# Kernel optimization log

Measured on AMD Instinct MI355X. Metric: run time of the kernel, lower is better.

Reference implementation:

```python
import jax, jax.numpy as jnp
import numpy as np


def setup_inputs() -> dict:
    key = jax.random.key(0)
    k1, k2 = jax.random.split(key)
    N, C, H, W = 8, 512, 64, 64
    K = 64
    x = jax.random.normal(k1, (N, C, H, W), dtype=jnp.float32)
    y = jax.random.normal(k2, (N, K, H, W), dtype=jnp.float32)
    scale = jnp.zeros((1,), dtype=jnp.float32)
    return {"x": x, "y": y, "scale": scale}


def reference(x, y, scale):
    N, C, H, W = x.shape
    K = y.shape[1]
    HW = H * W
    xq = x.reshape(N, C, HW)            # (N, C, HW) queries (channel-wise)
    yk = y.reshape(N, K, HW)            # (N, K, HW) keys/values
    # energy: (N, C, K)
    energy = jnp.einsum('ncs,nks->nck', xq, yk)
    # inverted max-subtraction: softmax(max_k(E) - E) over last dim
    energy_new = jnp.max(energy, axis=-1, keepdims=True) - energy
    attention = jax.nn.softmax(energy_new, axis=-1)  # (N, C, K)
    out = jnp.einsum('nck,nks->ncs', attention, yk)   # (N, C, HW)
    out = out.reshape(N, C, H, W)
    return x + scale * out
```

## Files before the change

### kernel.cpp

```cpp
#include <hip/hip_runtime.h>

#define N_ 8
#define C_ 512
#define K_ 64
#define HW_ 4096
#define SCHUNK 256
#define NCH 16

typedef __attribute__((ext_vector_type(8))) short short8;
typedef __attribute__((ext_vector_type(4))) float floatx4;

__device__ __forceinline__ short8 cvt8(const float* __restrict__ p){
  float4 u = *(const float4*)p;
  float4 w = *(const float4*)(p + 4);
  union { unsigned u32[4]; short8 s; } r;
  asm("v_cvt_pk_bf16_f32 %0, %1, %2" : "=v"(r.u32[0]) : "v"(u.x), "v"(u.y));
  asm("v_cvt_pk_bf16_f32 %0, %1, %2" : "=v"(r.u32[1]) : "v"(u.z), "v"(u.w));
  asm("v_cvt_pk_bf16_f32 %0, %1, %2" : "=v"(r.u32[2]) : "v"(w.x), "v"(w.y));
  asm("v_cvt_pk_bf16_f32 %0, %1, %2" : "=v"(r.u32[3]) : "v"(w.z), "v"(w.w));
  return r.s;
}

__device__ __forceinline__ void gload16(const void* g, void* l){
  __builtin_amdgcn_global_load_lds(
      (const __attribute__((address_space(1))) void*)g,
      (__attribute__((address_space(3))) void*)l, 16, 0, 0);
}

__global__ __launch_bounds__(256) void k_prep(const float* __restrict__ y,
                                              unsigned short* __restrict__ ybf,
                                              unsigned short* __restrict__ ytr){
  __shared__ unsigned short tile[64][72];
  int n  = blockIdx.x >> 6;
  int s0 = (blockIdx.x & 63) << 6;
  int tid = threadIdx.x;
  int k  = tid >> 2;
  int sc = (tid & 3) << 4;
  const float* yp = y + ((size_t)n * K_ + k) * HW_ + s0 + sc;
  union { unsigned short u16[16]; short8 s8[2]; uint4 q[2]; } u;
  u.s8[0] = cvt8(yp);
  u.s8[1] = cvt8(yp + 8);
  unsigned short* rp = ybf + ((size_t)n * K_ + k) * HW_ + s0 + sc;
  *(uint4*)rp       = u.q[0];
  *(uint4*)(rp + 8) = u.q[1];
#pragma unroll
  for (int j = 0; j < 16; ++j) tile[sc + j][k] = u.u16[j];
  __syncthreads();
  int s  = tid >> 2;
  int kc = (tid & 3) << 4;
  unsigned short* tp = ytr + ((size_t)n * HW_ + s0 + s) * K_ + kc;
  *(uint4*)tp       = *(const uint4*)&tile[s][kc];
  *(uint4*)(tp + 8) = *(const uint4*)&tile[s][kc + 8];
}

__global__ __launch_bounds__(1024) void k_fused(const float* __restrict__ x,
                                                const unsigned short* __restrict__ ybf,
                                                const unsigned short* __restrict__ ytr,
                                                const float* __restrict__ scale,
                                                float* __restrict__ out){
  __shared__ char smem[116736];

  const int bid = ((blockIdx.x & 7) << 5) | (blockIdx.x >> 3);
  const int ct = bid & 31, n = bid >> 5;
  const int tid = threadIdx.x;
  const int w = tid >> 6, l = tid & 63;
  const int lo = l & 15, hi = l >> 4;
  const int h = w >> 2, q = w & 3;
  const int c0 = ct << 4;

  float sc = scale[0];
  asm volatile("" :: "v"(sc));

  const char* asrc = (const char*)(x + ((size_t)n * C_ + c0 + w) * HW_)
                     + ((16 * l) ^ ((w & 7) << 4));
  const int kb = (w << 1) + (l >> 5);
  const char* bsrc0 = (const char*)(ybf + ((size_t)n * K_ + kb) * HW_)
                      + ((16 * (l & 31)) ^ ((kb & 7) << 4));
  const char* bsrc1 = bsrc0 + (size_t)32 * HW_ * 2;

  floatx4 acc = {0.f, 0.f, 0.f, 0.f};
  const int aswz = (lo & 7) << 4;
  const int brow = (q << 4) + lo;

#define AS(BUF) (smem + (BUF) * 49152)
#define BS(BUF) (smem + (BUF) * 49152 + 16384)
#define STAGE(BUF, CH)                                                         \
  {                                                                            \
    gload16(asrc  + (size_t)(CH) * (SCHUNK * 4), AS(BUF) + (w << 10));         \
    gload16(bsrc0 + (size_t)(CH) * (SCHUNK * 2), BS(BUF) + (w << 10));         \
    gload16(bsrc1 + (size_t)(CH) * (SCHUNK * 2), BS(BUF) + 16384 + (w << 10)); \
  }

  STAGE(0, 0)

#pragma unroll
  for (int ch = 0; ch < NCH; ++ch){
    const int cur = ch & 1;
    if (ch + 1 < NCH){
      STAGE(cur ^ 1, ch + 1)
      asm volatile("s_waitcnt vmcnt(3)" ::: "memory");
    } else {
      asm volatile("s_waitcnt vmcnt(0)" ::: "memory");
    }
    __builtin_amdgcn_s_barrier();
    __builtin_amdgcn_sched_barrier(0);
#pragma unroll
    for (int ss = 0; ss < 2; ++ss){
      int ao = (h << 8) + (ss << 7) + (hi << 5);
      const char* ab = AS(cur) + (lo << 10);
      float4 a0f = *(const float4*)(ab + ((ao     ) ^ aswz));
      float4 a1f = *(const float4*)(ab + ((ao + 16) ^ aswz));
      union { unsigned u32[4]; short8 s; } af;
      asm("v_cvt_pk_bf16_f32 %0, %1, %2" : "=v"(af.u32[0]) : "v"(a0f.x), "v"(a0f.y));
      asm("v_cvt_pk_bf16_f32 %0, %1, %2" : "=v"(af.u32[1]) : "v"(a0f.z), "v"(a0f.w));
      asm("v_cvt_pk_bf16_f32 %0, %1, %2" : "=v"(af.u32[2]) : "v"(a1f.x), "v"(a1f.y));
      asm("v_cvt_pk_bf16_f32 %0, %1, %2" : "=v"(af.u32[3]) : "v"(a1f.z), "v"(a1f.w));
      int bo = (h << 7) + (ss << 6) + (hi << 4);
      short8 bfr = *(const short8*)(BS(cur) + brow * 512 + (bo ^ aswz));
      acc = __builtin_amdgcn_mfma_f32_16x16x32_bf16(bfr, af.s, acc, 0, 0, 0);
    }
    __builtin_amdgcn_sched_barrier(0);
    __builtin_amdgcn_s_barrier();
  }
#undef STAGE

  float (*Els)[16][64] = (float (*)[16][64])(smem + 98304);
  *(floatx4*)&Els[h][lo][(q << 4) + (hi << 2)] = acc;
  __syncthreads();

  char* attl = smem + 114688;
  if (tid < 256){
    int c = tid >> 4, j = tid & 15;
    float4 t0 = *(const float4*)&Els[0][c][4 * j];
    float4 t1 = *(const float4*)&Els[1][c][4 * j];
    float4 t2 = *(const float4*)&Els[2][c][4 * j];
    float4 t3 = *(const float4*)&Els[3][c][4 * j];
    float e0 = t0.x + t1.x + t2.x + t3.x;
    float e1 = t0.y + t1.y + t2.y + t3.y;
    float e2 = t0.z + t1.z + t2.z + t3.z;
    float e3 = t0.w + t1.w + t2.w + t3.w;
    float m = fminf(fminf(e0, e1), fminf(e2, e3));
#pragma unroll
    for (int off = 8; off; off >>= 1) m = fminf(m, __shfl_xor(m, off, 16));
    float p0 = __expf(m - e0), p1 = __expf(m - e1);
    float p2 = __expf(m - e2), p3 = __expf(m - e3);
    float s = p0 + p1 + p2 + p3;
#pragma unroll
    for (int off = 8; off; off >>= 1) s += __shfl_xor(s, off, 16);
    float inv = 1.f / s;
    unsigned d0, d1;
    asm("v_cvt_pk_bf16_f32 %0, %1, %2" : "=v"(d0) : "v"(p0 * inv), "v"(p1 * inv));
    asm("v_cvt_pk_bf16_f32 %0, %1, %2" : "=v"(d1) : "v"(p2 * inv), "v"(p3 * inv));
    uint2 dd; dd.x = d0; dd.y = d1;
    *(uint2*)(attl + c * 128 + ((8 * j) ^ ((c & 7) << 4))) = dd;
  }
  __syncthreads();

  short8 batt0 = *(const short8*)(attl + lo * 128 + ((     hi * 16) ^ ((lo & 7) << 4)));
  short8 batt1 = *(const short8*)(attl + lo * 128 + ((64 + hi * 16) ^ ((lo & 7) << 4)));
  const unsigned short* ybn = ytr + (size_t)n * HW_ * K_;
  const int sP = w << 8;
  float (*Tw)[68] = (float (*)[68])(smem + w * 4352);
  size_t xb[4];
#pragma unroll
  for (int rg = 0; rg < 4; ++rg)
    xb[rg] = ((size_t)n * C_ + c0 + (rg << 2) + hi) * HW_ + sP + (lo << 2);

  short8 aA[8]; float4 xA[4];
  short8 aB[8]; float4 xB[4];

#define PVLOAD(G, AV, XV)                                                      \
  {                                                                            \
    int sg = sP + (G) * 64;                                                    \
    _Pragma("unroll")                                                          \
    for (int t = 0; t < 4; ++t){                                               \
      const unsigned short* ap = ybn + (size_t)(sg + t * 16 + lo) * K_ + (hi << 3); \
      AV[2 * t]     = *(const short8*)(ap);                                    \
      AV[2 * t + 1] = *(const short8*)(ap + 32);                               \
    }                                                                          \
    _Pragma("unroll")                                                          \
    for (int rg = 0; rg < 4; ++rg)                                             \
      XV[rg] = *(const float4*)(x + xb[rg] + (G) * 64);                        \
  }

#define PVCOMP(G, AV, XV)                                                      \
  {                                                                            \
    _Pragma("unroll")                                                          \
    for (int t = 0; t < 4; ++t){                                               \
      floatx4 a2 = {0.f, 0.f, 0.f, 0.f};                                       \
      a2 = __builtin_amdgcn_mfma_f32_16x16x32_bf16(AV[2 * t],     batt0, a2, 0, 0, 0); \
      a2 = __builtin_amdgcn_mfma_f32_16x16x32_bf16(AV[2 * t + 1], batt1, a2, 0, 0, 0); \
      *(floatx4*)&Tw[lo][t * 16 + (hi << 2)] = a2;    \
    }                                                                          \
    _Pragma("unroll")                                                          \
    for (int rg = 0; rg < 4; ++rg){                                            \
      float4 v  = *(const float4*)&Tw[(rg << 2) + hi][lo << 2];                \
      float4 xv = XV[rg];                                                      \
      float4 o;                                                                \
      o.x = xv.x + sc * v.x; o.y = xv.y + sc * v.y;                            \
      o.z = xv.z + sc * v.z; o.w = xv.w + sc * v.w;                            \
      *(float4*)(out + xb[rg] + (G) * 64) = o;                                 \
    }                                                                          \
  }

  PVLOAD(0, aA, xA)
  PVLOAD(1, aB, xB)
  PVCOMP(0, aA, xA)
  PVLOAD(2, aA, xA)
  PVCOMP(1, aB, xB)
  PVLOAD(3, aB, xB)
  PVCOMP(2, aA, xA)
  PVCOMP(3, aB, xB)
#undef PVLOAD
#undef PVCOMP
#undef AS
#undef BS
}

extern "C" void kernel_launch(void* const* d_in, const int* in_sizes, int n_in,
                              void* d_out, int out_size, void* d_ws, size_t ws_size,
                              hipStream_t stream){
  const float* x     = (const float*)d_in[0];
  const float* y     = (const float*)d_in[1];
  const float* scale = (const float*)d_in[2];
  float* out = (float*)d_out;

  char* ws = (char*)d_ws;
  unsigned short* ybf = (unsigned short*)(ws);
  unsigned short* ytr = (unsigned short*)(ws + (4u<<20));

  k_prep  <<<N_ * (HW_/64), 256,  0, stream>>>(y, ybf, ytr);
  k_fused <<<N_ * 32,       1024, 0, stream>>>(x, ybf, ytr, scale, out);
}
```

Baseline: 50.64 us.

## Split fused kernel into split-S energy/softmax kernel and separate PV kernel

Replaces the single 1024-thread fused kernel with a split-spatial energy kernel that accumulates partial C×K energies via global atomics, where the last-arriving block computes the softmax and writes bf16 attention to workspace. A separate PV kernel with more, smaller blocks then reads the attention and produces the output. The intent is more blocks and better occupancy across CUs. In exchange it adds a memset, atomics, an extra launch, and a second full read of x.

```diff
diff --git a/kernel.cpp b/kernel.cpp
--- a/kernel.cpp
+++ b/kernel.cpp
@@ -4,8 +4,10 @@
 #define C_ 512
 #define K_ 64
 #define HW_ 4096
-#define SCHUNK 256
-#define NCH 16
+#define NSP 4
+#define SRANGE (HW_ / NSP)
+#define SCHUNK 128
+#define NCH 8
 
 typedef __attribute__((ext_vector_type(8))) short short8;
 typedef __attribute__((ext_vector_type(4))) float floatx4;
@@ -53,42 +55,52 @@
   *(uint4*)(tp + 8) = *(const uint4*)&tile[s][kc + 8];
 }
 
-__global__ __launch_bounds__(1024) void k_fused(const float* __restrict__ x,
-                                                const unsigned short* __restrict__ ybf,
-                                                const unsigned short* __restrict__ ytr,
-                                                const float* __restrict__ scale,
-                                                float* __restrict__ out){
-  __shared__ char smem[116736];
-
-  const int bid = ((blockIdx.x & 7) << 5) | (blockIdx.x >> 3);
-  const int ct = bid & 31, n = bid >> 5;
+__global__ __launch_bounds__(256) void k_esm(const float* __restrict__ x,
+                                             const unsigned short* __restrict__ ybf,
+                                             float* __restrict__ eacc,
+                                             unsigned* __restrict__ cnt,
+                                             unsigned short* __restrict__ att){
+  __shared__ char smem[49152];
+  __shared__ unsigned tk;
+  const int bid = ((blockIdx.x & 7) << 7) | (blockIdx.x >> 3);
+  const int sp = bid & 3;
+  const int ct = (bid >> 2) & 31;
+  const int n  = bid >> 7;
   const int tid = threadIdx.x;
   const int w = tid >> 6, l = tid & 63;
   const int lo = l & 15, hi = l >> 4;
-  const int h = w >> 2, q = w & 3;
   const int c0 = ct << 4;
-
-  float sc = scale[0];
-  asm volatile("" :: "v"(sc));
-
-  const char* asrc = (const char*)(x + ((size_t)n * C_ + c0 + w) * HW_)
-                     + ((16 * l) ^ ((w & 7) << 4));
-  const int kb = (w << 1) + (l >> 5);
-  const char* bsrc0 = (const char*)(ybf + ((size_t)n * K_ + kb) * HW_)
-                      + ((16 * (l & 31)) ^ ((kb & 7) << 4));
-  const char* bsrc1 = bsrc0 + (size_t)32 * HW_ * 2;
-
-  floatx4 acc = {0.f, 0.f, 0.f, 0.f};
+  const int sb = sp * SRANGE;
+  const int pg = (n << 5) + ct;
+
+  const int ar0 = ((w << 1) + 0) * 2 + (l >> 5);
+  const int ar1 = ((w << 1) + 1) * 2 + (l >> 5);
+  const char* asrc0 = (const char*)(x + ((size_t)n * C_ + c0 + ar0) * HW_ + sb)
+                      + ((16 * (l & 31)) ^ ((ar0 & 7) << 4));
+  const char* asrc1 = (const char*)(x + ((size_t)n * C_ + c0 + ar1) * HW_ + sb)
+                      + ((16 * (l & 31)) ^ ((ar1 & 7) << 4));
+  const char* bsrc[4];
+#pragma unroll
+  for (int j = 0; j < 4; ++j){
+    int kk = ((w << 2) + j) * 4 + (l >> 4);
+    bsrc[j] = (const char*)(ybf + ((size_t)n * K_ + kk) * HW_ + sb)
+              + ((16 * (l & 15)) ^ ((kk & 7) << 4));
+  }
+
+  floatx4 acc[4];
+#pragma unroll
+  for (int q = 0; q < 4; ++q) acc[q] = (floatx4){0.f, 0.f, 0.f, 0.f};
   const int aswz = (lo & 7) << 4;
-  const int brow = (q << 4) + lo;
-
-#define AS(BUF) (smem + (BUF) * 49152)
-#define BS(BUF) (smem + (BUF) * 49152 + 16384)
+
+#define AS(BUF) (smem + (BUF) * 24576)
+#define BS(BUF) (smem + (BUF) * 24576 + 8192)
 #define STAGE(BUF, CH)                                                         \
   {                                                                            \
-    gload16(asrc  + (size_t)(CH) * (SCHUNK * 4), AS(BUF) + (w << 10));         \
-    gload16(bsrc0 + (size_t)(CH) * (SCHUNK * 2), BS(BUF) + (w << 10));         \
-    gload16(bsrc1 + (size_t)(CH) * (SCHUNK * 2), BS(BUF) + 16384 + (w << 10)); \
+    gload16(asrc0 + (size_t)(CH) * (SCHUNK * 4), AS(BUF) + (((w << 1) + 0) << 10)); \
+    gload16(asrc1 + (size_t)(CH) * (SCHUNK * 4), AS(BUF) + (((w << 1) + 1) << 10)); \
+    _Pragma("unroll")                                                          \
+    for (int j = 0; j < 4; ++j)                                                \
+      gload16(bsrc[j] + (size_t)(CH) * (SCHUNK * 2), BS(BUF) + (((w << 2) + j) << 10)); \
   }
 
   STAGE(0, 0)
@@ -98,16 +110,15 @@
     const int cur = ch & 1;
     if (ch + 1 < NCH){
       STAGE(cur ^ 1, ch + 1)
-      asm volatile("s_waitcnt vmcnt(3)" ::: "memory");
+      asm volatile("s_waitcnt vmcnt(6)" ::: "memory");
     } else {
       asm volatile("s_waitcnt vmcnt(0)" ::: "memory");
     }
     __builtin_amdgcn_s_barrier();
     __builtin_amdgcn_sched_barrier(0);
-#pragma unroll
-    for (int ss = 0; ss < 2; ++ss){
-      int ao = (h << 8) + (ss << 7) + (hi << 5);
-      const char* ab = AS(cur) + (lo << 10);
+    {
+      int ao = (w << 7) + (hi << 5);
+      const char* ab = AS(cur) + (lo << 9);
       float4 a0f = *(const float4*)(ab + ((ao     ) ^ aswz));
       float4 a1f = *(const float4*)(ab + ((ao + 16) ^ aswz));
       union { unsigned u32[4]; short8 s; } af;
@@ -115,30 +126,54 @@
       asm("v_cvt_pk_bf16_f32 %0, %1, %2" : "=v"(af.u32[1]) : "v"(a0f.z), "v"(a0f.w));
       asm("v_cvt_pk_bf16_f32 %0, %1, %2" : "=v"(af.u32[2]) : "v"(a1f.x), "v"(a1f.y));
       asm("v_cvt_pk_bf16_f32 %0, %1, %2" : "=v"(af.u32[3]) : "v"(a1f.z), "v"(a1f.w));
-      int bo = (h << 7) + (ss << 6) + (hi << 4);
-      short8 bfr = *(const short8*)(BS(cur) + brow * 512 + (bo ^ aswz));
-      acc = __builtin_amdgcn_mfma_f32_16x16x32_bf16(bfr, af.s, acc, 0, 0, 0);
+#pragma unroll
+      for (int q = 0; q < 4; ++q){
+        short8 b = *(const short8*)(BS(cur) + ((q << 4) + lo) * 256
+                                    + (((w << 6) + (hi << 4)) ^ aswz));
+        acc[q] = __builtin_amdgcn_mfma_f32_16x16x32_bf16(b, af.s, acc[q], 0, 0, 0);
+      }
     }
     __builtin_amdgcn_sched_barrier(0);
     __builtin_amdgcn_s_barrier();
   }
 #undef STAGE
 
-  float (*Els)[16][64] = (float (*)[16][64])(smem + 98304);
-  *(floatx4*)&Els[h][lo][(q << 4) + (hi << 2)] = acc;
-  __syncthreads();
-
-  char* attl = smem + 114688;
+  float (*Els)[16][64] = (float (*)[16][64])smem;
+#pragma unroll
+  for (int q = 0; q < 4; ++q)
+    *(floatx4*)&Els[w][lo][(q << 4) + (hi << 2)] = acc[q];
+  __syncthreads();
+
   if (tid < 256){
     int c = tid >> 4, j = tid & 15;
-    float4 t0 = *(const float4*)&Els[0][c][4 * j];
+    float4 e = *(const float4*)&Els[0][c][4 * j];
     float4 t1 = *(const float4*)&Els[1][c][4 * j];
     float4 t2 = *(const float4*)&Els[2][c][4 * j];
     float4 t3 = *(const float4*)&Els[3][c][4 * j];
-    float e0 = t0.x + t1.x + t2.x + t3.x;
-    float e1 = t0.y + t1.y + t2.y + t3.y;
-    float e2 = t0.z + t1.z + t2.z + t3.z;
-    float e3 = t0.w + t1.w + t2.w + t3.w;
+    e.x += t1.x + t2.x + t3.x; e.y += t1.y + t2.y + t3.y;
+    e.z += t1.z + t2.z + t3.z; e.w += t1.w + t2.w + t3.w;
+    float* dst = eacc + ((size_t)pg << 10) + (c << 6) + (j << 2);
+    atomicAdd(dst + 0, e.x);
+    atomicAdd(dst + 1, e.y);
+    atomicAdd(dst + 2, e.z);
+    atomicAdd(dst + 3, e.w);
+  }
+  __syncthreads();
+  if (tid == 0){
+    __threadfence();
+    tk = atomicAdd(&cnt[pg], 1u);
+  }
+  __syncthreads();
+  if (tk != NSP - 1) return;
+
+  __threadfence();
+  if (tid < 256){
+    int c = tid >> 4, j = tid & 15;
+    const float* src = eacc + ((size_t)pg << 10) + (c << 6) + (j << 2);
+    float e0 = __hip_atomic_load(src + 0, __ATOMIC_RELAXED, __HIP_MEMORY_SCOPE_AGENT);
+    float e1 = __hip_atomic_load(src + 1, __ATOMIC_RELAXED, __HIP_MEMORY_SCOPE_AGENT);
+    float e2 = __hip_atomic_load(src + 2, __ATOMIC_RELAXED, __HIP_MEMORY_SCOPE_AGENT);
+    float e3 = __hip_atomic_load(src + 3, __ATOMIC_RELAXED, __HIP_MEMORY_SCOPE_AGENT);
     float m = fminf(fminf(e0, e1), fminf(e2, e3));
 #pragma unroll
     for (int off = 8; off; off >>= 1) m = fminf(m, __shfl_xor(m, off, 16));
@@ -152,6 +187,33 @@
     asm("v_cvt_pk_bf16_f32 %0, %1, %2" : "=v"(d0) : "v"(p0 * inv), "v"(p1 * inv));
     asm("v_cvt_pk_bf16_f32 %0, %1, %2" : "=v"(d1) : "v"(p2 * inv), "v"(p3 * inv));
     uint2 dd; dd.x = d0; dd.y = d1;
+    *(uint2*)(att + ((size_t)n * C_ + c0 + c) * K_ + 4 * j) = dd;
+  }
+#undef AS
+#undef BS
+}
+
+__global__ __launch_bounds__(256) void k_pv(const float* __restrict__ x,
+                                            const unsigned short* __restrict__ att,
+                                            const unsigned short* __restrict__ ytr,
+                                            const float* __restrict__ scale,
+                                            float* __restrict__ out){
+  __shared__ float T[4][16][68];
+  __shared__ char attl[2048];
+  int bid = ((blockIdx.x & 7) << 8) | (blockIdx.x >> 3);
+  int sb = bid & 7;
+  int ct = (bid >> 3) & 31;
+  int n  = bid >> 8;
+  int tid = threadIdx.x;
+  int w  = tid >> 6;
+  int l  = tid & 63, lo = l & 15, hi = l >> 4;
+  int c0 = ct << 4;
+  int sP = (sb << 9) + (w << 7);
+  float sc = scale[0];
+
+  if (tid < 256){
+    int c = tid >> 4, j = tid & 15;
+    uint2 dd = *(const uint2*)(att + ((size_t)n * C_ + c0 + c) * K_ + 4 * j);
     *(uint2*)(attl + c * 128 + ((8 * j) ^ ((c & 7) << 4))) = dd;
   }
   __syncthreads();
@@ -159,8 +221,7 @@
   short8 batt0 = *(const short8*)(attl + lo * 128 + ((     hi * 16) ^ ((lo & 7) << 4)));
   short8 batt1 = *(const short8*)(attl + lo * 128 + ((64 + hi * 16) ^ ((lo & 7) << 4)));
   const unsigned short* ybn = ytr + (size_t)n * HW_ * K_;
-  const int sP = w << 8;
-  float (*Tw)[68] = (float (*)[68])(smem + w * 4352);
+  float (*Tw)[68] = T[w];
   size_t xb[4];
 #pragma unroll
   for (int rg = 0; rg < 4; ++rg)
@@ -206,15 +267,9 @@
   PVLOAD(0, aA, xA)
   PVLOAD(1, aB, xB)
   PVCOMP(0, aA, xA)
-  PVLOAD(2, aA, xA)
   PVCOMP(1, aB, xB)
-  PVLOAD(3, aB, xB)
-  PVCOMP(2, aA, xA)
-  PVCOMP(3, aB, xB)
 #undef PVLOAD
 #undef PVCOMP
-#undef AS
-#undef BS
 }
 
 extern "C" void kernel_launch(void* const* d_in, const int* in_sizes, int n_in,
@@ -226,9 +281,14 @@
   float* out = (float*)d_out;
 
   char* ws = (char*)d_ws;
-  unsigned short* ybf = (unsigned short*)(ws);
-  unsigned short* ytr = (unsigned short*)(ws + (4u<<20));
-
-  k_prep  <<<N_ * (HW_/64), 256,  0, stream>>>(y, ybf, ytr);
-  k_fused <<<N_ * 32,       1024, 0, stream>>>(x, ybf, ytr, scale, out);
-}
+  float*          eacc = (float*)(ws);
+  unsigned*       cnt  = (unsigned*)(ws + (1u<<20));
+  unsigned short* att  = (unsigned short*)(ws + (1u<<20) + 4096);
+  unsigned short* ybf  = (unsigned short*)(ws + (2u<<20));
+  unsigned short* ytr  = (unsigned short*)(ws + (6u<<20));
+
+  hipMemsetAsync(eacc, 0, (1u<<20) + 1024, stream);
+  k_prep <<<N_ * (HW_/64), 256, 0, stream>>>(y, ybf, ytr);
+  k_esm  <<<N_ * 32 * NSP, 256, 0, stream>>>(x, ybf, eacc, cnt, att);
+  k_pv   <<<N_ * 32 * 8,   256, 0, stream>>>(x, att, ytr, scale, out);
+}
```

Result: slower. 111.6 us (+120.3%).

## Make QK^T staging per-wave private to remove block-wide barriers

Applied to the files above, without the earlier changes.

Restructures the energy GEMM loop so each wave loads its own private slice of x and y into a per-wave LDS region. The block-level s_barrier pairs per chunk go away and each wave synchronises only through its own vmcnt waits. Chunks are halved to 128 elements with 32 iterations in a double-buffered ping-pong. This trades cross-wave data sharing, and possibly redundant loads, for the removal of workgroup-wide synchronisation stalls across 16 waves.

```diff
diff --git a/kernel.cpp b/kernel.cpp
--- a/kernel.cpp
+++ b/kernel.cpp
@@ -4,8 +4,8 @@
 #define C_ 512
 #define K_ 64
 #define HW_ 4096
-#define SCHUNK 256
-#define NCH 16
+#define SCHUNK 128
+#define NCH 32
 
 typedef __attribute__((ext_vector_type(8))) short short8;
 typedef __attribute__((ext_vector_type(4))) float floatx4;
@@ -71,58 +71,59 @@
   float sc = scale[0];
   asm volatile("" :: "v"(sc));
 
-  const char* asrc = (const char*)(x + ((size_t)n * C_ + c0 + w) * HW_)
-                     + ((16 * l) ^ ((w & 7) << 4));
-  const int kb = (w << 1) + (l >> 5);
-  const char* bsrc0 = (const char*)(ybf + ((size_t)n * K_ + kb) * HW_)
-                      + ((16 * (l & 31)) ^ ((kb & 7) << 4));
-  const char* bsrc1 = bsrc0 + (size_t)32 * HW_ * 2;
-
+  const int ar = l >> 3;
+  const int ag = (l & 7) ^ ar;
+  const char* asrc0 = (const char*)(x + ((size_t)n * C_ + c0 + 0 + ar) * HW_
+                                    + h * 32 + ag * 4);
+  const char* asrc1 = (const char*)(x + ((size_t)n * C_ + c0 + 8 + ar) * HW_
+                                    + h * 32 + ag * 4);
+  const int br = l >> 2;
+  const int bg = (l & 3) ^ (br & 3);
+  const char* bsrc = (const char*)(ybf + ((size_t)n * K_ + (q << 4) + br) * HW_
+                                   + h * 32 + bg * 8);
+
+  char* wbase = smem + w * 6144;
   floatx4 acc = {0.f, 0.f, 0.f, 0.f};
-  const int aswz = (lo & 7) << 4;
-  const int brow = (q << 4) + lo;
-
-#define AS(BUF) (smem + (BUF) * 49152)
-#define BS(BUF) (smem + (BUF) * 49152 + 16384)
-#define STAGE(BUF, CH)                                                         \
-  {                                                                            \
-    gload16(asrc  + (size_t)(CH) * (SCHUNK * 4), AS(BUF) + (w << 10));         \
-    gload16(bsrc0 + (size_t)(CH) * (SCHUNK * 2), BS(BUF) + (w << 10));         \
-    gload16(bsrc1 + (size_t)(CH) * (SCHUNK * 2), BS(BUF) + 16384 + (w << 10)); \
-  }
-
-  STAGE(0, 0)
-
-#pragma unroll
-  for (int ch = 0; ch < NCH; ++ch){
-    const int cur = ch & 1;
-    if (ch + 1 < NCH){
-      STAGE(cur ^ 1, ch + 1)
-      asm volatile("s_waitcnt vmcnt(3)" ::: "memory");
-    } else {
-      asm volatile("s_waitcnt vmcnt(0)" ::: "memory");
-    }
-    __builtin_amdgcn_s_barrier();
-    __builtin_amdgcn_sched_barrier(0);
-#pragma unroll
-    for (int ss = 0; ss < 2; ++ss){
-      int ao = (h << 8) + (ss << 7) + (hi << 5);
-      const char* ab = AS(cur) + (lo << 10);
-      float4 a0f = *(const float4*)(ab + ((ao     ) ^ aswz));
-      float4 a1f = *(const float4*)(ab + ((ao + 16) ^ aswz));
-      union { unsigned u32[4]; short8 s; } af;
-      asm("v_cvt_pk_bf16_f32 %0, %1, %2" : "=v"(af.u32[0]) : "v"(a0f.x), "v"(a0f.y));
-      asm("v_cvt_pk_bf16_f32 %0, %1, %2" : "=v"(af.u32[1]) : "v"(a0f.z), "v"(a0f.w));
-      asm("v_cvt_pk_bf16_f32 %0, %1, %2" : "=v"(af.u32[2]) : "v"(a1f.x), "v"(a1f.y));
-      asm("v_cvt_pk_bf16_f32 %0, %1, %2" : "=v"(af.u32[3]) : "v"(a1f.z), "v"(a1f.w));
-      int bo = (h << 7) + (ss << 6) + (hi << 4);
-      short8 bfr = *(const short8*)(BS(cur) + brow * 512 + (bo ^ aswz));
-      acc = __builtin_amdgcn_mfma_f32_16x16x32_bf16(bfr, af.s, acc, 0, 0, 0);
-    }
-    __builtin_amdgcn_sched_barrier(0);
-    __builtin_amdgcn_s_barrier();
-  }
-#undef STAGE
+
+#define ESTG(BUF, CH)                                                          \
+  {                                                                            \
+    gload16(asrc0 + (size_t)(CH) * (SCHUNK * 4), wbase + (BUF) * 3072);        \
+    gload16(asrc1 + (size_t)(CH) * (SCHUNK * 4), wbase + (BUF) * 3072 + 1024); \
+    gload16(bsrc  + (size_t)(CH) * (SCHUNK * 2), wbase + (BUF) * 3072 + 2048); \
+  }
+
+#define ECMP(BUF)                                                              \
+  {                                                                            \
+    const char* Ab = wbase + (BUF) * 3072;                                     \
+    float4 f0 = *(const float4*)(Ab + lo * 128 + (((hi << 1)       ^ (lo & 7)) << 4)); \
+    float4 f1 = *(const float4*)(Ab + lo * 128 + ((((hi << 1) | 1) ^ (lo & 7)) << 4)); \
+    union { unsigned u32[4]; short8 s; } xf;                                   \
+    asm("v_cvt_pk_bf16_f32 %0, %1, %2" : "=v"(xf.u32[0]) : "v"(f0.x), "v"(f0.y)); \
+    asm("v_cvt_pk_bf16_f32 %0, %1, %2" : "=v"(xf.u32[1]) : "v"(f0.z), "v"(f0.w)); \
+    asm("v_cvt_pk_bf16_f32 %0, %1, %2" : "=v"(xf.u32[2]) : "v"(f1.x), "v"(f1.y)); \
+    asm("v_cvt_pk_bf16_f32 %0, %1, %2" : "=v"(xf.u32[3]) : "v"(f1.z), "v"(f1.w)); \
+    short8 yf = *(const short8*)(Ab + 2048 + lo * 64 + ((hi ^ (lo & 3)) << 4)); \
+       \
+    acc = __builtin_amdgcn_mfma_f32_16x16x32_bf16(yf, xf.s, acc, 0, 0, 0);     \
+  }
+
+  ESTG(0, 0) ESTG(1, 1)
+
+  for (int cp = 0; cp < 15; ++cp){
+    int ch = cp << 1;
+    asm volatile("s_waitcnt vmcnt(3)" ::: "memory");
+    ECMP(0)
+    ESTG(0, ch + 2)
+    asm volatile("s_waitcnt vmcnt(3)" ::: "memory");
+    ECMP(1)
+    ESTG(1, ch + 3)
+  }
+  asm volatile("s_waitcnt vmcnt(3)" ::: "memory");
+  ECMP(0)
+  asm volatile("s_waitcnt vmcnt(0)" ::: "memory");
+  ECMP(1)
+#undef ESTG
+#undef ECMP
 
   float (*Els)[16][64] = (float (*)[16][64])(smem + 98304);
   *(floatx4*)&Els[h][lo][(q << 4) + (hi << 2)] = acc;
@@ -213,8 +214,6 @@
   PVCOMP(3, aB, xB)
 #undef PVLOAD
 #undef PVCOMP
-#undef AS
-#undef BS
 }
 
 extern "C" void kernel_launch(void* const* d_in, const int* in_sizes, int n_in,
```

Result: faster. 49.00 us (-3.2%).
